# Optimization experiments

Measured on AMD Instinct MI355X. Metric: run time of the kernel, lower is better.

The kernel has to match this reference:

```python
import jax, jax.numpy as jnp
import numpy as np

B, C, H, W = 2, 256, 48, 48
KS = 5
HEADS = 4
DH = 64
OC = HEADS * DH
SCALE = DH ** -0.5


def setup_inputs() -> dict:
    key = jax.random.key(0)
    k1, k2, k3, k4, k5 = jax.random.split(key, 5)
    kvmap1 = jax.random.normal(k1, (B, C, H, W), dtype=jnp.float32)
    qmap = jax.random.normal(k2, (B, C, H, W), dtype=jnp.float32)
    kvmap2 = jax.random.normal(k3, (B, C, H, W), dtype=jnp.float32)
    Wq = jax.random.normal(k4, (OC, C), dtype=jnp.float32) * 0.02
    Wkv = jax.random.normal(k5, (OC, C), dtype=jnp.float32) * 0.02
    return {"kvmap1": kvmap1, "qmap": qmap, "kvmap2": kvmap2, "Wq": Wq, "Wkv": Wkv}


def reference(kvmap1, qmap, kvmap2, Wq, Wkv):
    b, c, h, w = qmap.shape
    ks = KS
    pad_lo, pad_hi = ks // 2, (ks - 1) // 2
    pad = ((0, 0), (0, 0), (pad_lo, pad_hi), (pad_lo, pad_hi))
    p1 = jnp.pad(kvmap1, pad)
    p2 = jnp.pad(kvmap2, pad)
    kv = jnp.stack([p1, p2], axis=-1)  # [b, c, Hp, Wp, 2]

    # 1x1 Conv3d (pointwise over channels); note k and v share the same projection,
    # so k == v in the original module -- compute once.
    kmap = jnp.einsum('bchwl,oc->bohwl', kv, Wkv)  # [b, oc, Hp, Wp, 2]
    q = jnp.einsum('bchw,oc->bohw', qmap, Wq)      # [b, oc, h, w]

    # local windows (im2col): window flat order is (l, k1, k2), l outermost
    kw = jnp.stack(
        [kmap[:, :, i:i + h, j:j + w, :] for i in range(ks) for j in range(ks)],
        axis=-1,
    )  # [b, oc, h, w, 2, ks*ks]
    kw = kw.reshape(b, HEADS, DH, h, w, 2 * ks * ks)
    kw = kw.transpose(0, 1, 3, 4, 5, 2).reshape(b, HEADS, h * w, 2 * ks * ks, DH)

    qh = q.reshape(b, HEADS, DH, h * w).transpose(0, 1, 3, 2) * SCALE  # [b, n, x, d]
    logits = jnp.einsum('bnxd,bnxyd->bnxy', qh, kw)
    weights = jax.nn.softmax(logits, axis=-1)
    attn = jnp.einsum('bnxy,bnxyd->bnxd', weights, kw)  # v == k
    out = attn.transpose(0, 1, 3, 2).reshape(b, HEADS * DH, h, w)
    return out
```

## Files before the change

kernel.cpp:

```cpp
#include <hip/hip_runtime.h>

#define HH 48
#define WWD 48
#define CC 256
#define OCC 256
#define NPIX 2304
#define NB 2
#define NHEADS 4
#define DHEAD 64
#define SCALE_E 0.1803368802f

#define TH 2
#define TW 16
#define PHR 6
#define PWC 20
#define NPOS 120
#define NTILES 72

#define SLAB ((size_t)NPIX * OCC)

typedef __attribute__((ext_vector_type(8))) short short8v;
typedef __attribute__((ext_vector_type(4))) float floatx4;

__device__ __forceinline__ unsigned short f2bf(float f) {
    union { float f; unsigned u; } v; v.f = f;
    unsigned r = v.u + 0x7FFFu + ((v.u >> 16) & 1u);
    return (unsigned short)(r >> 16);
}
__device__ __forceinline__ float bf2f(unsigned short b) {
    union { unsigned u; float f; } v; v.u = ((unsigned)b) << 16; return v.f;
}

__device__ __forceinline__ float xreduce8(float s) {
    s += __int_as_float(__builtin_amdgcn_update_dpp(
        0, __float_as_int(s), 0xB1, 0xf, 0xf, true));
    s += __int_as_float(__builtin_amdgcn_update_dpp(
        0, __float_as_int(s), 0x4E, 0xf, 0xf, true));
    s += __shfl_xor(s, 4, 64);
    return s;
}

__global__ __launch_bounds__(256) void proj_mfma(
    const float* __restrict__ Wq, const float* __restrict__ Wkv,
    const float* __restrict__ qmap, const float* __restrict__ kv1,
    const float* __restrict__ kv2, unsigned short* __restrict__ ws)
{
    __shared__ unsigned short Bs[64 * 64];

    const int z = blockIdx.z;
    const int map = z % 3;
    const int b = z / 3;
    const float* Wmat = (map == 0) ? Wq : Wkv;
    const float* X = ((map == 0) ? qmap : (map == 1) ? kv1 : kv2)
                     + (size_t)b * CC * NPIX;
    unsigned short* out = ws + ((size_t)map * NB + b) * SLAB;

    const int tid = threadIdx.x;
    const int x0 = blockIdx.x * 64;
    const int o0 = blockIdx.y * 64;
    const int lane = tid & 63;
    const int wv = tid >> 6;
    const int l15 = lane & 15;
    const int l4 = lane >> 4;
    const int kq_w = tid >> 4;
    const int xq = tid & 15;

    const float* Arow = Wmat + (size_t)(o0 + wv * 16 + l15) * CC;

    floatx4 acc[4];
#pragma unroll
    for (int nt = 0; nt < 4; ++nt) acc[nt] = (floatx4){0.f, 0.f, 0.f, 0.f};

#pragma unroll
    for (int kt = 0; kt < 4; ++kt) {
        const int k0t = kt * 64;

        float4 av0 = *reinterpret_cast<const float4*>(Arow + k0t + l4 * 8);
        float4 av1 = *reinterpret_cast<const float4*>(Arow + k0t + l4 * 8 + 4);
        float4 av2 = *reinterpret_cast<const float4*>(Arow + k0t + 32 + l4 * 8);
        float4 av3 = *reinterpret_cast<const float4*>(Arow + k0t + 32 + l4 * 8 + 4);

        float4 xv[4];
#pragma unroll
        for (int i = 0; i < 4; ++i)
            xv[i] = *reinterpret_cast<const float4*>(
                &X[(size_t)(k0t + kq_w * 4 + i) * NPIX + x0 + xq * 4]);
        {
            float xt[4][4] = {
                {xv[0].x, xv[1].x, xv[2].x, xv[3].x},
                {xv[0].y, xv[1].y, xv[2].y, xv[3].y},
                {xv[0].z, xv[1].z, xv[2].z, xv[3].z},
                {xv[0].w, xv[1].w, xv[2].w, xv[3].w}};
#pragma unroll
            for (int j = 0; j < 4; ++j) {
                const int x = xq * 4 + j;
                ushort4 u;
                u.x = f2bf(xt[j][0]); u.y = f2bf(xt[j][1]);
                u.z = f2bf(xt[j][2]); u.w = f2bf(xt[j][3]);
                *reinterpret_cast<ushort4*>(
                    (char*)Bs + x * 128 + ((kq_w ^ (x & 15)) << 3)) = u;
            }
        }
        __syncthreads();

#pragma unroll
        for (int kc = 0; kc < 2; ++kc) {
            const float4 va = (kc == 0) ? av0 : av2;
            const float4 vb = (kc == 0) ? av1 : av3;
            const float a[8] = {va.x, va.y, va.z, va.w, vb.x, vb.y, vb.z, vb.w};
            short8v ah, al;
#pragma unroll
            for (int j = 0; j < 8; ++j) {
                const unsigned short h = f2bf(a[j]);
                ah[j] = (short)h;
                al[j] = (short)f2bf(a[j] - bf2f(h));
            }
#pragma unroll
            for (int nt = 0; nt < 4; ++nt) {
                const int x = nt * 16 + l15;
                const int kq = kc * 8 + l4 * 2;
                ushort4 b0 = *reinterpret_cast<ushort4*>(
                    (char*)Bs + x * 128 + ((kq ^ l15) << 3));
                ushort4 b1 = *reinterpret_cast<ushort4*>(
                    (char*)Bs + x * 128 + (((kq + 1) ^ l15) << 3));
                short8v bh;
                bh[0] = (short)b0.x; bh[1] = (short)b0.y;
                bh[2] = (short)b0.z; bh[3] = (short)b0.w;
                bh[4] = (short)b1.x; bh[5] = (short)b1.y;
                bh[6] = (short)b1.z; bh[7] = (short)b1.w;
                acc[nt] = __builtin_amdgcn_mfma_f32_16x16x32_bf16(ah, bh, acc[nt], 0, 0, 0);
                acc[nt] = __builtin_amdgcn_mfma_f32_16x16x32_bf16(al, bh, acc[nt], 0, 0, 0);
            }
        }
        __syncthreads();
    }

#pragma unroll
    for (int nt = 0; nt < 4; ++nt) {
        const int x = nt * 16 + l15;
        ushort4 u;
        u.x = f2bf(acc[nt][0]); u.y = f2bf(acc[nt][1]);
        u.z = f2bf(acc[nt][2]); u.w = f2bf(acc[nt][3]);
        *reinterpret_cast<ushort4*>(
            &out[(size_t)(x0 + x) * OCC + o0 + wv * 16 + l4 * 4]) = u;
    }
}

__global__ __launch_bounds__(256, 4) void attn_kernel(
    const unsigned short* __restrict__ ws, float* __restrict__ out)
{
    __shared__ __align__(16) unsigned short kp[2 * NPOS * 64];

    const int tid = threadIdx.x;
    const int bid = blockIdx.x;
    const int tile = bid % NTILES;
    const int head = (bid / NTILES) % NHEADS;
    const int b = bid / (NTILES * NHEADS);
    const int h0 = (tile / 3) * TH;
    const int w0 = (tile % 3) * TW;

    const unsigned short* qp = ws + (size_t)(0 * NB + b) * SLAB;
    const unsigned short* k1 = ws + (size_t)(1 * NB + b) * SLAB;
    const unsigned short* k2 = ws + (size_t)(2 * NB + b) * SLAB;
    const int co = head * DHEAD;

#pragma unroll
    for (int it = 0; it < 8; ++it) {
        const int g = it * 256 + tid;
        if (g < 2 * NPOS * 8) {
            const int row = g >> 3;
            const int u = g & 7;
            const int lm = row >= NPOS;
            const int pos = row - (lm ? NPOS : 0);
            const int pr = pos / PWC, pc = pos - pr * PWC;
            const int hh = h0 + pr - 2, wp = w0 + pc - 2;
            short8v v = {0, 0, 0, 0, 0, 0, 0, 0};
            if (hh >= 0 && hh < HH && wp >= 0 && wp < WWD) {
                const unsigned short* kmap = lm ? k2 : k1;
                v = *reinterpret_cast<const short8v*>(
                    &kmap[(size_t)(hh * WWD + wp) * OCC + co
                          + ((u ^ (pos & 7)) << 3)]);
            }
            *reinterpret_cast<short8v*>(&kp[row * 64 + u * 8]) = v;
        }
    }
    __syncthreads();

    const int e = tid & 7;
    const int pixl = tid >> 3;
    const int pi = pixl >> 4, pj = pixl & 15;
    const int pix = (h0 + pi) * WWD + (w0 + pj);

    float qd[8];
    {
        short8v qv = *reinterpret_cast<const short8v*>(
            &qp[(size_t)pix * OCC + co + e * 8]);
#pragma unroll
        for (int k = 0; k < 8; ++k)
            qd[k] = bf2f((unsigned short)qv[k]) * SCALE_E;
    }

    float den = 0.f;
    float acc[8];
#pragma unroll
    for (int k = 0; k < 8; ++k) acc[k] = 0.f;

#pragma unroll
    for (int r = 0; r < 25; ++r) {
        const int di = r / 5, dj = r % 5;
        const int pos = (pi + di) * PWC + (pj + dj);
        const int uoff = ((e ^ (pos & 7)) << 3);

        short8v ku1 = *reinterpret_cast<const short8v*>(&kp[pos * 64 + uoff]);
        short8v ku2 = *reinterpret_cast<const short8v*>(
            &kp[(NPOS + pos) * 64 + uoff]);

        float k1f[8], k2f[8];
#pragma unroll
        for (int k = 0; k < 8; ++k) {
            k1f[k] = bf2f((unsigned short)ku1[k]);
            k2f[k] = bf2f((unsigned short)ku2[k]);
        }

        float s1 = 0.f, s2 = 0.f;
#pragma unroll
        for (int k = 0; k < 8; ++k) {
            s1 += qd[k] * k1f[k];
            s2 += qd[k] * k2f[k];
        }
        s1 = xreduce8(s1);
        s2 = xreduce8(s2);

        const float p1 = exp2f(s1);
        const float p2 = exp2f(s2);
        den += p1 + p2;
#pragma unroll
        for (int k = 0; k < 8; ++k)
            acc[k] += p1 * k1f[k] + p2 * k2f[k];
    }

    const float rden = 1.f / den;

#pragma unroll
    for (int k = 0; k < 8; ++k) {
        out[((size_t)b * OCC + co + e * 8 + k) * NPIX + pix] = acc[k] * rden;
    }
}

extern "C" void kernel_launch(void* const* d_in, const int* in_sizes, int n_in,
                              void* d_out, int out_size, void* d_ws, size_t ws_size,
                              hipStream_t stream) {
    const float* kvmap1 = (const float*)d_in[0];
    const float* qmap   = (const float*)d_in[1];
    const float* kvmap2 = (const float*)d_in[2];
    const float* Wq     = (const float*)d_in[3];
    const float* Wkv    = (const float*)d_in[4];
    float* out = (float*)d_out;
    unsigned short* ws = (unsigned short*)d_ws;

    dim3 ggrid(NPIX / 64, OCC / 64, 3 * NB);
    proj_mfma<<<ggrid, 256, 0, stream>>>(Wq, Wkv, qmap, kvmap1, kvmap2, ws);

    const int nblocks = NTILES * NHEADS * NB;
    attn_kernel<<<nblocks, 256, 0, stream>>>(ws, out);
}
```

Measured before the change: 33.79 us.

## Pre-split weights, store projections as fp16, use packed fdot2 in attention

Adds a small kernel that splits Wq/Wkv into bf16 hi/lo halves once per call, so the projection kernel loads bf16 weights instead of converting fp32 in every block. The projection uses hardware packed bf16 conversion for inputs and now writes fp16 (round-toward-zero) projections instead of bf16. The attention kernel reads these as half2 and uses fdot2 for the q·k dot products, and remaps block indices to interleave tiles across heads and batch. This trades an extra kernel launch and fp16 range/precision risk for fewer ALU conversion instructions.

```diff
diff --git a/kernel.cpp b/kernel.cpp
--- a/kernel.cpp
+++ b/kernel.cpp
@@ -18,9 +18,13 @@
 #define NTILES 72
 
 #define SLAB ((size_t)NPIX * OCC)
+#define WQN (256 * 256)
 
 typedef __attribute__((ext_vector_type(8))) short short8v;
 typedef __attribute__((ext_vector_type(4))) float floatx4;
+typedef _Float16 half2v __attribute__((ext_vector_type(2)));
+typedef __fp16 fp16x2 __attribute__((ext_vector_type(2)));
+union h2u { unsigned u; half2v h; fp16x2 g; };
 
 __device__ __forceinline__ unsigned short f2bf(float f) {
     union { float f; unsigned u; } v; v.f = f;
@@ -29,6 +33,11 @@
 }
 __device__ __forceinline__ float bf2f(unsigned short b) {
     union { unsigned u; float f; } v; v.u = ((unsigned)b) << 16; return v.f;
+}
+__device__ __forceinline__ unsigned cvt_pk_bf16(float a, float b) {
+    unsigned r;
+    asm("v_cvt_pk_bf16_f32 %0, %1, %2" : "=v"(r) : "v"(a), "v"(b));
+    return r;
 }
 
 __device__ __forceinline__ float xreduce8(float s) {
@@ -40,19 +49,46 @@
     return s;
 }
 
+__global__ __launch_bounds__(256) void prep_w(
+    const float* __restrict__ Wq, const float* __restrict__ Wkv,
+    unsigned short* __restrict__ wsW)
+{
+    const int g = blockIdx.x * 256 + threadIdx.x;
+    const int mat = g >> 13;
+    const int i = (g & 8191) * 8;
+    const float* W = mat ? Wkv : Wq;
+    unsigned short* hi = wsW + (size_t)mat * 2 * WQN;
+    unsigned short* lo = hi + WQN;
+
+    float4 a = *reinterpret_cast<const float4*>(&W[i]);
+    float4 b = *reinterpret_cast<const float4*>(&W[i + 4]);
+    const float v[8] = {a.x, a.y, a.z, a.w, b.x, b.y, b.z, b.w};
+    unsigned short hv[8], lv[8];
+#pragma unroll
+    for (int k = 0; k < 8; ++k) {
+        hv[k] = f2bf(v[k]);
+        lv[k] = f2bf(v[k] - bf2f(hv[k]));
+    }
+    *reinterpret_cast<ushort4*>(&hi[i]) = make_ushort4(hv[0], hv[1], hv[2], hv[3]);
+    *reinterpret_cast<ushort4*>(&hi[i + 4]) = make_ushort4(hv[4], hv[5], hv[6], hv[7]);
+    *reinterpret_cast<ushort4*>(&lo[i]) = make_ushort4(lv[0], lv[1], lv[2], lv[3]);
+    *reinterpret_cast<ushort4*>(&lo[i + 4]) = make_ushort4(lv[4], lv[5], lv[6], lv[7]);
+}
+
 __global__ __launch_bounds__(256) void proj_mfma(
-    const float* __restrict__ Wq, const float* __restrict__ Wkv,
     const float* __restrict__ qmap, const float* __restrict__ kv1,
-    const float* __restrict__ kv2, unsigned short* __restrict__ ws)
+    const float* __restrict__ kv2, const unsigned short* __restrict__ wsW,
+    unsigned short* __restrict__ ws)
 {
     __shared__ unsigned short Bs[64 * 64];
 
     const int z = blockIdx.z;
     const int map = z % 3;
     const int b = z / 3;
-    const float* Wmat = (map == 0) ? Wq : Wkv;
     const float* X = ((map == 0) ? qmap : (map == 1) ? kv1 : kv2)
                      + (size_t)b * CC * NPIX;
+    const unsigned short* Whi = wsW + (size_t)(map == 0 ? 0 : 1) * 2 * WQN;
+    const unsigned short* Wlo = Whi + WQN;
     unsigned short* out = ws + ((size_t)map * NB + b) * SLAB;
 
     const int tid = threadIdx.x;
@@ -65,7 +101,7 @@
     const int kq_w = tid >> 4;
     const int xq = tid & 15;
 
-    const float* Arow = Wmat + (size_t)(o0 + wv * 16 + l15) * CC;
+    const int arowO = o0 + wv * 16 + l15;
 
     floatx4 acc[4];
 #pragma unroll
@@ -74,11 +110,12 @@
 #pragma unroll
     for (int kt = 0; kt < 4; ++kt) {
         const int k0t = kt * 64;
-
-        float4 av0 = *reinterpret_cast<const float4*>(Arow + k0t + l4 * 8);
-        float4 av1 = *reinterpret_cast<const float4*>(Arow + k0t + l4 * 8 + 4);
-        float4 av2 = *reinterpret_cast<const float4*>(Arow + k0t + 32 + l4 * 8);
-        float4 av3 = *reinterpret_cast<const float4*>(Arow + k0t + 32 + l4 * 8 + 4);
+        const int abase = arowO * CC + k0t + l4 * 8;
+
+        short8v ah0 = *reinterpret_cast<const short8v*>(Whi + abase);
+        short8v al0 = *reinterpret_cast<const short8v*>(Wlo + abase);
+        short8v ah1 = *reinterpret_cast<const short8v*>(Whi + abase + 32);
+        short8v al1 = *reinterpret_cast<const short8v*>(Wlo + abase + 32);
 
         float4 xv[4];
 #pragma unroll
@@ -94,27 +131,19 @@
 #pragma unroll
             for (int j = 0; j < 4; ++j) {
                 const int x = xq * 4 + j;
-                ushort4 u;
-                u.x = f2bf(xt[j][0]); u.y = f2bf(xt[j][1]);
-                u.z = f2bf(xt[j][2]); u.w = f2bf(xt[j][3]);
-                *reinterpret_cast<ushort4*>(
-                    (char*)Bs + x * 128 + ((kq_w ^ (x & 15)) << 3)) = u;
+                const unsigned w0 = cvt_pk_bf16(xt[j][0], xt[j][1]);
+                const unsigned w1 = cvt_pk_bf16(xt[j][2], xt[j][3]);
+                *reinterpret_cast<uint2*>(
+                    (char*)Bs + x * 128 + ((kq_w ^ (x & 15)) << 3)) =
+                    make_uint2(w0, w1);
             }
         }
         __syncthreads();
 
 #pragma unroll
         for (int kc = 0; kc < 2; ++kc) {
-            const float4 va = (kc == 0) ? av0 : av2;
-            const float4 vb = (kc == 0) ? av1 : av3;
-            const float a[8] = {va.x, va.y, va.z, va.w, vb.x, vb.y, vb.z, vb.w};
-            short8v ah, al;
-#pragma unroll
-            for (int j = 0; j < 8; ++j) {
-                const unsigned short h = f2bf(a[j]);
-                ah[j] = (short)h;
-                al[j] = (short)f2bf(a[j] - bf2f(h));
-            }
+            const short8v ah = kc ? ah1 : ah0;
+            const short8v al = kc ? al1 : al0;
 #pragma unroll
             for (int nt = 0; nt < 4; ++nt) {
                 const int x = nt * 16 + l15;
@@ -138,11 +167,12 @@
 #pragma unroll
     for (int nt = 0; nt < 4; ++nt) {
         const int x = nt * 16 + l15;
-        ushort4 u;
-        u.x = f2bf(acc[nt][0]); u.y = f2bf(acc[nt][1]);
-        u.z = f2bf(acc[nt][2]); u.w = f2bf(acc[nt][3]);
-        *reinterpret_cast<ushort4*>(
-            &out[(size_t)(x0 + x) * OCC + o0 + wv * 16 + l4 * 4]) = u;
+        h2u p0, p1;
+        p0.g = __builtin_amdgcn_cvt_pkrtz(acc[nt][0], acc[nt][1]);
+        p1.g = __builtin_amdgcn_cvt_pkrtz(acc[nt][2], acc[nt][3]);
+        *reinterpret_cast<uint2*>(
+            &out[(size_t)(x0 + x) * OCC + o0 + wv * 16 + l4 * 4]) =
+            make_uint2(p0.u, p1.u);
     }
 }
 
@@ -152,7 +182,8 @@
     __shared__ __align__(16) unsigned short kp[2 * NPOS * 64];
 
     const int tid = threadIdx.x;
-    const int bid = blockIdx.x;
+    const int bid0 = blockIdx.x;
+    const int bid = (bid0 & 7) * 72 + (bid0 >> 3);
     const int tile = bid % NTILES;
     const int head = (bid / NTILES) % NHEADS;
     const int b = bid / (NTILES * NHEADS);
@@ -191,13 +222,16 @@
     const int pi = pixl >> 4, pj = pixl & 15;
     const int pix = (h0 + pi) * WWD + (w0 + pj);
 
-    float qd[8];
+    half2v qs[4];
     {
-        short8v qv = *reinterpret_cast<const short8v*>(
+        uint4 qw = *reinterpret_cast<const uint4*>(
             &qp[(size_t)pix * OCC + co + e * 8]);
-#pragma unroll
-        for (int k = 0; k < 8; ++k)
-            qd[k] = bf2f((unsigned short)qv[k]) * SCALE_E;
+        const half2v sc2 = {(_Float16)SCALE_E, (_Float16)SCALE_E};
+        h2u t;
+        t.u = qw.x; qs[0] = t.h * sc2;
+        t.u = qw.y; qs[1] = t.h * sc2;
+        t.u = qw.z; qs[2] = t.h * sc2;
+        t.u = qw.w; qs[3] = t.h * sc2;
     }
 
     float den = 0.f;
@@ -211,32 +245,38 @@
         const int pos = (pi + di) * PWC + (pj + dj);
         const int uoff = ((e ^ (pos & 7)) << 3);
 
-        short8v ku1 = *reinterpret_cast<const short8v*>(&kp[pos * 64 + uoff]);
-        short8v ku2 = *reinterpret_cast<const short8v*>(
+        uint4 k1w = *reinterpret_cast<const uint4*>(&kp[pos * 64 + uoff]);
+        uint4 k2w = *reinterpret_cast<const uint4*>(
             &kp[(NPOS + pos) * 64 + uoff]);
 
-        float k1f[8], k2f[8];
-#pragma unroll
-        for (int k = 0; k < 8; ++k) {
-            k1f[k] = bf2f((unsigned short)ku1[k]);
-            k2f[k] = bf2f((unsigned short)ku2[k]);
-        }
+        h2u a0, a1, a2, a3, c0, c1, c2, c3;
+        a0.u = k1w.x; a1.u = k1w.y; a2.u = k1w.z; a3.u = k1w.w;
+        c0.u = k2w.x; c1.u = k2w.y; c2.u = k2w.z; c3.u = k2w.w;
 
         float s1 = 0.f, s2 = 0.f;
-#pragma unroll
-        for (int k = 0; k < 8; ++k) {
-            s1 += qd[k] * k1f[k];
-            s2 += qd[k] * k2f[k];
-        }
+        s1 = __builtin_amdgcn_fdot2(a0.h, qs[0], s1, false);
+        s1 = __builtin_amdgcn_fdot2(a1.h, qs[1], s1, false);
+        s1 = __builtin_amdgcn_fdot2(a2.h, qs[2], s1, false);
+        s1 = __builtin_amdgcn_fdot2(a3.h, qs[3], s1, false);
+        s2 = __builtin_amdgcn_fdot2(c0.h, qs[0], s2, false);
+        s2 = __builtin_amdgcn_fdot2(c1.h, qs[1], s2, false);
+        s2 = __builtin_amdgcn_fdot2(c2.h, qs[2], s2, false);
+        s2 = __builtin_amdgcn_fdot2(c3.h, qs[3], s2, false);
         s1 = xreduce8(s1);
         s2 = xreduce8(s2);
 
         const float p1 = exp2f(s1);
         const float p2 = exp2f(s2);
         den += p1 + p2;
-#pragma unroll
-        for (int k = 0; k < 8; ++k)
-            acc[k] += p1 * k1f[k] + p2 * k2f[k];
+
+        acc[0] += p1 * (float)a0.h[0] + p2 * (float)c0.h[0];
+        acc[1] += p1 * (float)a0.h[1] + p2 * (float)c0.h[1];
+        acc[2] += p1 * (float)a1.h[0] + p2 * (float)c1.h[0];
+        acc[3] += p1 * (float)a1.h[1] + p2 * (float)c1.h[1];
+        acc[4] += p1 * (float)a2.h[0] + p2 * (float)c2.h[0];
+        acc[5] += p1 * (float)a2.h[1] + p2 * (float)c2.h[1];
+        acc[6] += p1 * (float)a3.h[0] + p2 * (float)c3.h[0];
+        acc[7] += p1 * (float)a3.h[1] + p2 * (float)c3.h[1];
     }
 
     const float rden = 1.f / den;
@@ -257,9 +297,12 @@
     const float* Wkv    = (const float*)d_in[4];
     float* out = (float*)d_out;
     unsigned short* ws = (unsigned short*)d_ws;
+    unsigned short* wsW = ws + 6 * SLAB;
+
+    prep_w<<<64, 256, 0, stream>>>(Wq, Wkv, wsW);
 
     dim3 ggrid(NPIX / 64, OCC / 64, 3 * NB);
-    proj_mfma<<<ggrid, 256, 0, stream>>>(Wq, Wkv, qmap, kvmap1, kvmap2, ws);
+    proj_mfma<<<ggrid, 256, 0, stream>>>(qmap, kvmap1, kvmap2, wsW, ws);
 
     const int nblocks = NTILES * NHEADS * NB;
     attn_kernel<<<nblocks, 256, 0, stream>>>(ws, out);
```

Result: slower. 38.66 us (+14.4%).
